# Kernel optimization log

Hardware: AMD Instinct MI355X
Metric: run time of the kernel (lower is better)

The kernel has to match this reference:

```python
import jax, jax.numpy as jnp
import numpy as np

H = W = 512
K = 16          # max instance id (ids 1..K; 0 = background)
N_SIGMA = 1
FG_W = 1.0
W_INST, W_VAR, W_SEED = 1.0, 10.0, 1.0


def _xym(h, w, dtype):
    # torch: linspace(0,1,512) grids, sliced to [:, :h, :w]
    x = jnp.linspace(0.0, 1.0, 512)[:w]
    y = jnp.linspace(0.0, 1.0, 512)[:h]
    xm = jnp.broadcast_to(x[None, :], (h, w))
    ym = jnp.broadcast_to(y[:, None], (h, w))
    return jnp.stack([xm, ym], 0).astype(dtype)  # [2,h,w]


def _lovasz_hinge(logits, labels):
    # logits, labels: flat [P]; labels in {0,1} float
    signs = 2.0 * labels - 1.0
    errors = 1.0 - logits * signs
    perm = jnp.argsort(-errors)           # descending sort
    errors_sorted = errors[perm]
    gt_sorted = labels[perm]
    gts = gt_sorted.sum()
    inter = gts - jnp.cumsum(gt_sorted)
    union = gts + jnp.cumsum(1.0 - gt_sorted)
    jac = 1.0 - inter / union
    grad = jnp.concatenate([jac[:1], jac[1:] - jac[:-1]])
    # lovasz grad is computed from .data (detached) in the torch impl
    return jnp.dot(jax.nn.relu(errors_sorted), jax.lax.stop_gradient(grad))


def _per_instance(mask, spatial_emb, sigma, seed, xym):
    # mask: [H,W] float {0,1}; spatial_emb: [2,H,W]; sigma: [n_sigma,H,W]; seed: [H,W]
    cnt = mask.sum()
    safe = jnp.maximum(cnt, 1.0)
    center = jnp.sum(xym * mask, (1, 2)) / safe                        # [2] (to_center=True)
    s = jnp.sum(sigma * mask, (1, 2)) / safe                           # [n_sigma]
    var = jnp.sum((sigma - jax.lax.stop_gradient(s)[:, None, None]) ** 2 * mask) / (N_SIGMA * safe)
    s_exp = jnp.exp(s * 10.0)
    dist = jnp.exp(-jnp.sum((spatial_emb - center[:, None, None]) ** 2 * s_exp[:, None, None], 0))  # [H,W]
    inst = _lovasz_hinge(dist.ravel() * 2.0 - 1.0, mask.ravel())
    seed_l = FG_W * jnp.sum((seed - jax.lax.stop_gradient(dist)) ** 2 * mask)
    present = cnt > 0
    z = jnp.zeros((), dist.dtype)
    return (jnp.where(present, var, z), jnp.where(present, inst, z),
            jnp.where(present, seed_l, z), present.astype(dist.dtype))


def _per_image(pred, inst, lab, xym):
    spatial_emb = jnp.tanh(pred[0:2]) + xym                            # [2,H,W]
    sigma = pred[2:2 + N_SIGMA]                                        # [n_sigma,H,W]
    seed = jax.nn.sigmoid(pred[2 + N_SIGMA])                           # [H,W]
    ids = jnp.arange(1, K + 1)
    masks = (inst[None] == ids[:, None, None]).astype(pred.dtype)      # [K,H,W]
    var, instl, seedl, pres = jax.vmap(
        _per_instance, in_axes=(0, None, None, None, None))(masks, spatial_emb, sigma, seed, xym)
    obj = pres.sum()
    safe_obj = jnp.maximum(obj, 1.0)
    bg = (lab == 0).astype(pred.dtype)
    seed_total = (jnp.sum(seed ** 2 * bg) + seedl.sum()) / float(H * W)
    return W_INST * instl.sum() / safe_obj + W_VAR * var.sum() / safe_obj + W_SEED * seed_total


def setup_inputs() -> dict:
    key = jax.random.key(0)
    k1, k2, k3 = jax.random.split(key, 3)
    prediction = jax.random.normal(k1, (8, 4, H, W), dtype=jnp.float32)
    instances = jax.random.randint(k2, (8, H, W), 0, K + 1, dtype=jnp.int32)
    labels = jax.random.randint(k3, (8, H, W), 0, 2, dtype=jnp.int32)
    return {"prediction": prediction, "instances": instances, "labels": labels}


def reference(prediction, instances, labels):
    xym = _xym(prediction.shape[2], prediction.shape[3], prediction.dtype)
    losses = jax.vmap(_per_image, in_axes=(0, 0, 0, None))(prediction, instances, labels, xym)
    return losses.mean() + prediction.sum() * 0.0
```

## Files before the change

kernel.cpp:

```cpp
#include <hip/hip_runtime.h>

#define HH 512
#define WW 512
#define NPIX (HH*WW)
#define KK 16
#define BB 8
#define NB 192
#define NBP 200
#define CHS 128
#define CHV 256

__device__ __forceinline__ float fast_rcp(float x){ return __builtin_amdgcn_rcpf(x); }
__device__ __forceinline__ float fast_tanh(float x){
  x = fminf(fmaxf(x, -15.f), 15.f);
  float t = __expf(2.f*x);
  return (t-1.f)*fast_rcp(t+1.f);
}
__device__ __forceinline__ float fast_sigmoid(float x){
  x = fminf(fmaxf(x, -30.f), 30.f);
  return fast_rcp(1.f+__expf(-x));
}

__device__ __forceinline__ float dpp_row_sum16(float v){
  v += __int_as_float(__builtin_amdgcn_update_dpp(0, __float_as_int(v), 0x111, 0xf, 0xf, true));
  v += __int_as_float(__builtin_amdgcn_update_dpp(0, __float_as_int(v), 0x112, 0xf, 0xf, true));
  v += __int_as_float(__builtin_amdgcn_update_dpp(0, __float_as_int(v), 0x114, 0xf, 0xf, true));
  v += __int_as_float(__builtin_amdgcn_update_dpp(0, __float_as_int(v), 0x118, 0xf, 0xf, true));
  return v;
}

__global__ void __launch_bounds__(256) k_sums(
    const float* __restrict__ pred, const int* __restrict__ inst,
    const int* __restrict__ lab, float* __restrict__ partial_s ,
    float* __restrict__ partial_b ) {
  const int bid = blockIdx.x;
  const int b  = bid & 7;
  const int ch = bid >> 3;
  const int tid = threadIdx.x;
  const int wave = tid >> 6, lane = tid & 63;
  __shared__ float lred[KK][16][5];
  __shared__ float lbg[4];
  const float inv = 1.f/511.f;
  const float* ps = pred + (size_t)b*4*NPIX + 2*NPIX;
  const float* pd = ps + NPIX;
  const int*   ib = inst + (size_t)b*NPIX;
  const int*   lb = lab  + (size_t)b*NPIX;
  const int p = ch*2048 + tid*8;
  int4   iv0 = *(const int4*)(ib + p),     iv1 = *(const int4*)(ib + p + 4);
  int4   lv0 = *(const int4*)(lb + p),     lv1 = *(const int4*)(lb + p + 4);
  float4 sv0 = *(const float4*)(ps + p),   sv1 = *(const float4*)(ps + p + 4);
  float4 dv0 = *(const float4*)(pd + p),   dv1 = *(const float4*)(pd + p + 4);
  const float ym  = (float)(p >> 9) * inv;
  const float xm0 = (float)(p & (WW-1)) * inv;
  int   ida[8] = {iv0.x, iv0.y, iv0.z, iv0.w, iv1.x, iv1.y, iv1.z, iv1.w};
  int   laa[8] = {lv0.x, lv0.y, lv0.z, lv0.w, lv1.x, lv1.y, lv1.z, lv1.w};
  float sga[8] = {sv0.x, sv0.y, sv0.z, sv0.w, sv1.x, sv1.y, sv1.z, sv1.w};
  float sda[8] = {dv0.x, dv0.y, dv0.z, dv0.w, dv1.x, dv1.y, dv1.z, dv1.w};
  float xja[8], sg2[8];
  #pragma unroll
  for (int j = 0; j < 8; ++j) {
    xja[j] = xm0 + (float)j*inv;
    sg2[j] = sga[j]*sga[j];
  }

  float sbg = 0.f;
  #pragma unroll
  for (int j = 0; j < 8; ++j)
    if (laa[j] == 0) { float sd = fast_sigmoid(sda[j]); sbg += sd*sd; }
  #pragma unroll
  for (int off = 32; off; off >>= 1) sbg += __shfl_down(sbg, off);
  if (lane == 0) lbg[wave] = sbg;

  #pragma unroll
  for (int k = 0; k < KK; ++k) {
    float c = 0.f, sx = 0.f, ss = 0.f, sq = 0.f;
    #pragma unroll
    for (int j = 0; j < 8; ++j) {
      float m = (ida[j] == k+1) ? 1.f : 0.f;
      c  += m;
      sx = fmaf(m, xja[j], sx);
      ss = fmaf(m, sga[j], ss);
      sq = fmaf(m, sg2[j], sq);
    }
    float sy = c * ym;
    c  = dpp_row_sum16(c);
    sx = dpp_row_sum16(sx);
    sy = dpp_row_sum16(sy);
    ss = dpp_row_sum16(ss);
    sq = dpp_row_sum16(sq);
    if ((lane & 15) == 15) {
      int g = wave*4 + (lane >> 4);
      lred[k][g][0] = c;  lred[k][g][1] = sx; lred[k][g][2] = sy;
      lred[k][g][3] = ss; lred[k][g][4] = sq;
    }
  }
  __syncthreads();
  if (tid < KK) {
    #pragma unroll
    for (int comp = 0; comp < 5; ++comp) {
      float a = 0.f;
      #pragma unroll
      for (int g = 0; g < 16; ++g) a += lred[tid][g][comp];
      partial_s[((size_t)b*80 + tid*5 + comp)*CHS + ch] = a;
    }
  }
  if (tid == 64) partial_b[bid] = lbg[0] + lbg[1] + lbg[2] + lbg[3];
}

__global__ void __launch_bounds__(128) k_reduce(
    const float* __restrict__ partial_s, float* __restrict__ der) {
  const int seg = blockIdx.x;
  const int b = seg >> 4, k = seg & 15;
  const int tid = threadIdx.x;
  const int w = tid >> 6, l = tid & 63;
  __shared__ float red5[5][2];
  #pragma unroll
  for (int comp = 0; comp < 5; ++comp) {
    const float* row = partial_s + ((size_t)b*80 + k*5 + comp)*CHS;
    float a = row[tid];
    #pragma unroll
    for (int off = 32; off; off >>= 1) a += __shfl_down(a, off);
    if (l == 0) red5[comp][w] = a;
  }
  __syncthreads();
  if (tid == 0) {
    float cnt = red5[0][0]+red5[0][1];
    float sx  = red5[1][0]+red5[1][1];
    float sy  = red5[2][0]+red5[2][1];
    float ss  = red5[3][0]+red5[3][1];
    float sq  = red5[4][0]+red5[4][1];
    float safe = fmaxf(cnt, 1.f);
    float rs = fast_rcp(safe);
    float sb = ss*rs;
    float* dd = der + seg*8;
    dd[0] = sx*rs; dd[1] = sy*rs;
    dd[2] = __expf(10.f*sb);
    dd[3] = (cnt > 0.f) ? 1.f : 0.f;
    dd[4] = sb;
    dd[5] = cnt;
    dd[6] = sq - cnt*sb*sb;
  }
}

__global__ void __launch_bounds__(256, 4) k_hist(
    const float* __restrict__ pred, const int* __restrict__ inst,
    const float* __restrict__ der, unsigned int* __restrict__ hist,
    float* __restrict__ partial_v ) {
  const int bid = blockIdx.x;
  const int b  = bid & 7;
  const int ch = bid >> 3;
  const int tid = threadIdx.x;
  const int g = tid >> 4, l4 = tid & 15;
  __shared__ unsigned int lh[KK][NBP];
  __shared__ float sder[KK][4];
  __shared__ float lsl[4];
  if (tid < KK) {
    const float* dd = der + (b*KK + tid)*8;
    sder[tid][0] = dd[0]; sder[tid][1] = dd[1]; sder[tid][2] = dd[2];
  }
  for (int i = tid; i < KK*NBP; i += 256) ((unsigned int*)lh)[i] = 0u;
  __syncthreads();
  float cxa[KK], cya[KK], sea[KK];
  #pragma unroll
  for (int k = 0; k < KK; ++k) {
    cxa[k] = sder[k][0]; cya[k] = sder[k][1]; sea[k] = sder[k][2];
  }
  const float inv = 1.f/511.f;
  const float* pbx = pred + (size_t)b*4*NPIX;
  const float* pby = pbx + NPIX;
  const float* pbd = pbx + 3*NPIX;
  const int*   ib  = inst + (size_t)b*NPIX;
  const int p = ch*1024 + g*64 + l4*4;
  float4 px = *(const float4*)(pbx + p);
  float4 py = *(const float4*)(pby + p);
  int4   iv = *(const int4*)(ib + p);
  float4 dv = *(const float4*)(pbd + p);
  const float ym  = (float)(p >> 9) * inv;
  const float xm0 = (float)(p & (WW-1)) * inv;
  float pxa[4] = {px.x, px.y, px.z, px.w};
  float pya[4] = {py.x, py.y, py.z, py.w};
  int   ida[4] = {iv.x, iv.y, iv.z, iv.w};
  float sda[4] = {dv.x, dv.y, dv.z, dv.w};
  float sloss = 0.f;
  #pragma unroll
  for (int j = 0; j < 4; ++j) {
    float sex = fast_tanh(pxa[j]) + xm0 + (float)j*inv;
    float sey = fast_tanh(pya[j]) + ym;
    int id = ida[j];
    float down = 0.f;
    #pragma unroll
    for (int k = 0; k < KK; ++k) {
      float dx = sex - cxa[k], dy = sey - cya[k];
      float d = __expf(-sea[k]*(dx*dx + dy*dy));
      bool fg = (id == k+1);
      float u  = fg ? (1.f - d) : d;
      int bkt = (int)(u * (float)NB);
      bkt = bkt < (NB-1) ? bkt : (NB-1);
      atomicAdd(&lh[k][bkt], fg ? 0x10001u : 1u);
      down = fg ? d : down;
    }
    if (id >= 1) {
      float dsee = fast_sigmoid(sda[j]) - down;
      sloss = fmaf(dsee, dsee, sloss);
    }
  }
  __syncthreads();
  #pragma unroll
  for (int k = 0; k < KK; ++k) {
    unsigned int* gh = hist + ((size_t)(b*KK + k)*CHV + ch)*NB;
    if (tid < NB) gh[tid] = lh[k][tid];
  }
  #pragma unroll
  for (int off = 32; off; off >>= 1) sloss += __shfl_down(sloss, off);
  if ((tid & 63) == 0) lsl[tid >> 6] = sloss;
  __syncthreads();
  if (tid == 0) partial_v[bid] = lsl[0] + lsl[1] + lsl[2] + lsl[3];
}

__global__ void __launch_bounds__(256) k_lovasz(
    const unsigned int* __restrict__ hist, const float* __restrict__ der,
    const float* __restrict__ partial_v, const float* __restrict__ partial_b,
    float* __restrict__ instl, unsigned int* __restrict__ done,
    float* __restrict__ out) {
  const int seg = blockIdx.x;
  const int tid = threadIdx.x;
  __shared__ float nbL[NB], fbL[NB];
  __shared__ unsigned int sOld;
  const float gts = der[seg*8 + 5];
  const unsigned int* h = hist + (size_t)seg*CHV*NB;
  if (tid < NB) {
    unsigned int nlo = 0, nhi = 0;
    #pragma unroll 8
    for (int c = 0; c < CHV; ++c) {
      unsigned int v = h[(size_t)c*NB + tid];
      nlo += v & 0xffffu; nhi += v >> 16;
    }
    nbL[tid] = (float)nlo; fbL[tid] = (float)nhi;
  }
  __syncthreads();
  if (tid < 64) {
    const int lane = tid;
    float lsum = 0.f;
    if (gts > 0.f) {
      float carryN = 0.f, carryF = 0.f;
      #pragma unroll
      for (int it = 0; it < NB/64; ++it) {
        int bkt = NB - 1 - (it*64 + lane);
        float nb = nbL[bkt], fb = fbL[bkt];
        float sn = nb, sf = fb;
        #pragma unroll
        for (int off = 1; off < 64; off <<= 1) {
          float tn = __shfl_up(sn, off);
          float tf = __shfl_up(sf, off);
          if (lane >= off) { sn += tn; sf += tf; }
        }
        float Nb = carryN + sn - nb;
        float Fb = carryF + sf - fb;
        if (nb > 0.f) {
          float e  = ((float)bkt + 0.5f) * (2.0f/(float)NB);
          float j0 = 1.f - (gts - Fb) / (gts + Nb - Fb);
          float N1 = Nb + nb, F1 = Fb + fb;
          float j1 = 1.f - (gts - F1) / (gts + N1 - F1);
          lsum += e * (j1 - j0);
        }
        carryN += __shfl(sn, 63);
        carryF += __shfl(sf, 63);
      }
      #pragma unroll
      for (int off = 32; off; off >>= 1) lsum += __shfl_down(lsum, off);
    }
    if (lane == 0) {
      instl[seg] = lsum;
      __threadfence();
      sOld = atomicAdd(done, 1u);
    }
  }
  __syncthreads();
  if ((sOld & 127u) != 127u) return;
  __threadfence();
  __shared__ float vtmp[256], btmp[256];
  {
    const int b8 = tid >> 5, j = tid & 31;
    float a = 0.f, c = 0.f;
    #pragma unroll
    for (int i = 0; i < 8; ++i) a += partial_v[(size_t)(j + 32*i)*8 + b8];
    #pragma unroll
    for (int i = 0; i < 4; ++i) c += partial_b[(size_t)(j + 32*i)*8 + b8];
    vtmp[tid] = a; btmp[tid] = c;
  }
  __syncthreads();
  float myv = 0.f;
  if (tid < BB) {
    int b = tid;
    float svl = 0.f, sbg = 0.f;
    #pragma unroll
    for (int j = 0; j < 32; ++j) { svl += vtmp[b*32 + j]; sbg += btmp[b*32 + j]; }
    float obj = 0.f, il = 0.f, vr = 0.f;
    for (int k = 0; k < KK; ++k) {
      int s2 = b*KK + k;
      float cnt = der[s2*8 + 5];
      if (cnt > 0.f) {
        obj += 1.f;
        il  += instl[s2];
        vr  += der[s2*8 + 6] / cnt;
      }
    }
    float so = fmaxf(obj, 1.f);
    myv = il/so + 10.f*vr/so + (sbg + svl)/(float)NPIX;
  }
  #pragma unroll
  for (int off = 4; off; off >>= 1) myv += __shfl_down(myv, off);
  if (tid == 0) out[0] = myv * (1.f/(float)BB);
}

extern "C" void kernel_launch(void* const* d_in, const int* in_sizes, int n_in,
                              void* d_out, int out_size, void* d_ws, size_t ws_size,
                              hipStream_t stream) {
  const float* pred = (const float*)d_in[0];
  const int*   inst = (const int*)d_in[1];
  const int*   lab  = (const int*)d_in[2];
  float* out = (float*)d_out;

  float* der        = (float*)d_ws;
  float* instl      = (float*)((char*)d_ws + 4160);
  unsigned int* done= (unsigned int*)((char*)d_ws + 4736);
  float* partial_b  = (float*)((char*)d_ws + 8192);
  float* partial_v  = (float*)((char*)d_ws + 16384);
  float* partial_s  = (float*)((char*)d_ws + 24576);
  unsigned int* hist= (unsigned int*)((char*)d_ws + 679936);

  k_sums  <<<BB*CHS, 256, 0, stream>>>(pred, inst, lab, partial_s, partial_b);
  k_reduce<<<BB*KK, 128, 0, stream>>>(partial_s, der);
  k_hist  <<<BB*CHV, 256, 0, stream>>>(pred, inst, der, hist, partial_v);
  k_lovasz<<<BB*KK, 256, 0, stream>>>(hist, der, partial_v, partial_b,
                                      instl, done, out);
}
```

Baseline: 61.17 us.

## Fuse reduce into sums via last-block, atomically merge histograms, algebraic exp2 distance

The per-instance reduction kernel is folded into k_sums: the last block to finish, detected with an atomic counter, computes the derived centers and scales, which removes one launch. Per-block histograms are no longer written out in full. k_hist instead merges non-zero bins into one global 64-bit histogram per segment with atomics, and that histogram is zeroed inside k_sums. The lovasz kernel therefore reads 192 bins per segment instead of reducing 256 chunks. The distance exponent is expanded into precomputed coefficients with exp2, and bucketing uses a pre-scaled value. The risks are atomic contention, a serial last-block reduction over 128 chunks, and small numeric differences from the expanded quadratic.

```diff
diff --git a/kernel.cpp b/kernel.cpp
--- a/kernel.cpp
+++ b/kernel.cpp
@@ -32,7 +32,9 @@
 __global__ void __launch_bounds__(256) k_sums(
     const float* __restrict__ pred, const int* __restrict__ inst,
     const int* __restrict__ lab, float* __restrict__ partial_s ,
-    float* __restrict__ partial_b ) {
+    float* __restrict__ partial_b ,
+    unsigned long long* __restrict__ hist64, unsigned int* __restrict__ done2,
+    float* __restrict__ der) {
   const int bid = blockIdx.x;
   const int b  = bid & 7;
   const int ch = bid >> 3;
@@ -40,6 +42,8 @@
   const int wave = tid >> 6, lane = tid & 63;
   __shared__ float lred[KK][16][5];
   __shared__ float lbg[4];
+  __shared__ unsigned int sOld2;
+  if (tid < 48) ((unsigned int*)hist64)[bid*48 + tid] = 0u;
   const float inv = 1.f/511.f;
   const float* ps = pred + (size_t)b*4*NPIX + 2*NPIX;
   const float* pd = ps + NPIX;
@@ -105,46 +109,38 @@
     }
   }
   if (tid == 64) partial_b[bid] = lbg[0] + lbg[1] + lbg[2] + lbg[3];
-}
-
-__global__ void __launch_bounds__(128) k_reduce(
-    const float* __restrict__ partial_s, float* __restrict__ der) {
-  const int seg = blockIdx.x;
-  const int b = seg >> 4, k = seg & 15;
-  const int tid = threadIdx.x;
-  const int w = tid >> 6, l = tid & 63;
-  __shared__ float red5[5][2];
-  #pragma unroll
-  for (int comp = 0; comp < 5; ++comp) {
-    const float* row = partial_s + ((size_t)b*80 + k*5 + comp)*CHS;
-    float a = row[tid];
-    #pragma unroll
-    for (int off = 32; off; off >>= 1) a += __shfl_down(a, off);
-    if (l == 0) red5[comp][w] = a;
-  }
-  __syncthreads();
-  if (tid == 0) {
-    float cnt = red5[0][0]+red5[0][1];
-    float sx  = red5[1][0]+red5[1][1];
-    float sy  = red5[2][0]+red5[2][1];
-    float ss  = red5[3][0]+red5[3][1];
-    float sq  = red5[4][0]+red5[4][1];
+  __syncthreads();
+  if (tid == 0) { __threadfence(); sOld2 = atomicAdd(done2, 1u); }
+  __syncthreads();
+  if ((sOld2 & 1023u) != 1023u) return;
+  __threadfence();
+  if (tid < 128) {
+    const int seg = tid, b2 = seg >> 4, k2 = seg & 15;
+    float acc[5];
+    #pragma unroll
+    for (int comp = 0; comp < 5; ++comp) {
+      const float* row = partial_s + ((size_t)b2*80 + k2*5 + comp)*CHS;
+      float a = 0.f;
+      for (int c2 = 0; c2 < CHS; ++c2) a += row[c2];
+      acc[comp] = a;
+    }
+    float cnt = acc[0];
     float safe = fmaxf(cnt, 1.f);
     float rs = fast_rcp(safe);
-    float sb = ss*rs;
+    float sb = acc[3]*rs;
     float* dd = der + seg*8;
-    dd[0] = sx*rs; dd[1] = sy*rs;
+    dd[0] = acc[1]*rs; dd[1] = acc[2]*rs;
     dd[2] = __expf(10.f*sb);
     dd[3] = (cnt > 0.f) ? 1.f : 0.f;
     dd[4] = sb;
     dd[5] = cnt;
-    dd[6] = sq - cnt*sb*sb;
+    dd[6] = acc[4] - cnt*sb*sb;
   }
 }
 
 __global__ void __launch_bounds__(256, 4) k_hist(
     const float* __restrict__ pred, const int* __restrict__ inst,
-    const float* __restrict__ der, unsigned int* __restrict__ hist,
+    const float* __restrict__ der, unsigned long long* __restrict__ hist64,
     float* __restrict__ partial_v ) {
   const int bid = blockIdx.x;
   const int b  = bid & 7;
@@ -160,10 +156,16 @@
   }
   for (int i = tid; i < KK*NBP; i += 256) ((unsigned int*)lh)[i] = 0u;
   __syncthreads();
-  float cxa[KK], cya[KK], sea[KK];
+  const float L2E = 1.4426950408889634f;
+  float seaL[KK], AL[KK], BL[KK], CL[KK];
   #pragma unroll
   for (int k = 0; k < KK; ++k) {
-    cxa[k] = sder[k][0]; cya[k] = sder[k][1]; sea[k] = sder[k][2];
+    float cx = sder[k][0], cy = sder[k][1], se = sder[k][2];
+    float seL = se * L2E;
+    seaL[k] = -seL;
+    AL[k] = 2.f*cx*seL;
+    BL[k] = 2.f*cy*seL;
+    CL[k] = -(cx*cx + cy*cy)*seL;
   }
   const float inv = 1.f/511.f;
   const float* pbx = pred + (size_t)b*4*NPIX;
@@ -186,15 +188,17 @@
   for (int j = 0; j < 4; ++j) {
     float sex = fast_tanh(pxa[j]) + xm0 + (float)j*inv;
     float sey = fast_tanh(pya[j]) + ym;
+    float s2 = fmaf(sex, sex, sey*sey);
     int id = ida[j];
     float down = 0.f;
     #pragma unroll
     for (int k = 0; k < KK; ++k) {
-      float dx = sex - cxa[k], dy = sey - cya[k];
-      float d = __expf(-sea[k]*(dx*dx + dy*dy));
+      float t2 = fmaf(seaL[k], s2, fmaf(AL[k], sex, fmaf(BL[k], sey, CL[k])));
+      float d = __builtin_amdgcn_exp2f(t2);
       bool fg = (id == k+1);
-      float u  = fg ? (1.f - d) : d;
-      int bkt = (int)(u * (float)NB);
+      float dN = d * (float)NB;
+      float uN = fg ? ((float)NB - dN) : dN;
+      int bkt = (int)uN;
       bkt = bkt < (NB-1) ? bkt : (NB-1);
       atomicAdd(&lh[k][bkt], fg ? 0x10001u : 1u);
       down = fg ? d : down;
@@ -207,8 +211,14 @@
   __syncthreads();
   #pragma unroll
   for (int k = 0; k < KK; ++k) {
-    unsigned int* gh = hist + ((size_t)(b*KK + k)*CHV + ch)*NB;
-    if (tid < NB) gh[tid] = lh[k][tid];
+    if (tid < NB) {
+      unsigned int v = lh[k][tid];
+      if (v) {
+        unsigned long long add = (unsigned long long)(v & 0xffffu)
+                               | ((unsigned long long)(v >> 16) << 32);
+        atomicAdd(&hist64[(size_t)(b*KK + k)*NB + tid], add);
+      }
+    }
   }
   #pragma unroll
   for (int off = 32; off; off >>= 1) sloss += __shfl_down(sloss, off);
@@ -218,26 +228,15 @@
 }
 
 __global__ void __launch_bounds__(256) k_lovasz(
-    const unsigned int* __restrict__ hist, const float* __restrict__ der,
+    const unsigned long long* __restrict__ hist64, const float* __restrict__ der,
     const float* __restrict__ partial_v, const float* __restrict__ partial_b,
     float* __restrict__ instl, unsigned int* __restrict__ done,
     float* __restrict__ out) {
   const int seg = blockIdx.x;
   const int tid = threadIdx.x;
-  __shared__ float nbL[NB], fbL[NB];
   __shared__ unsigned int sOld;
   const float gts = der[seg*8 + 5];
-  const unsigned int* h = hist + (size_t)seg*CHV*NB;
-  if (tid < NB) {
-    unsigned int nlo = 0, nhi = 0;
-    #pragma unroll 8
-    for (int c = 0; c < CHV; ++c) {
-      unsigned int v = h[(size_t)c*NB + tid];
-      nlo += v & 0xffffu; nhi += v >> 16;
-    }
-    nbL[tid] = (float)nlo; fbL[tid] = (float)nhi;
-  }
-  __syncthreads();
+  const unsigned long long* h = hist64 + (size_t)seg*NB;
   if (tid < 64) {
     const int lane = tid;
     float lsum = 0.f;
@@ -246,7 +245,9 @@
       #pragma unroll
       for (int it = 0; it < NB/64; ++it) {
         int bkt = NB - 1 - (it*64 + lane);
-        float nb = nbL[bkt], fb = fbL[bkt];
+        unsigned long long v = h[bkt];
+        float nb = (float)(unsigned int)(v & 0xffffffffu);
+        float fb = (float)(unsigned int)(v >> 32);
         float sn = nb, sf = fb;
         #pragma unroll
         for (int off = 1; off < 64; off <<= 1) {
@@ -321,17 +322,18 @@
   const int*   lab  = (const int*)d_in[2];
   float* out = (float*)d_out;
 
-  float* der        = (float*)d_ws;
-  float* instl      = (float*)((char*)d_ws + 4160);
-  unsigned int* done= (unsigned int*)((char*)d_ws + 4736);
-  float* partial_b  = (float*)((char*)d_ws + 8192);
-  float* partial_v  = (float*)((char*)d_ws + 16384);
-  float* partial_s  = (float*)((char*)d_ws + 24576);
-  unsigned int* hist= (unsigned int*)((char*)d_ws + 679936);
-
-  k_sums  <<<BB*CHS, 256, 0, stream>>>(pred, inst, lab, partial_s, partial_b);
-  k_reduce<<<BB*KK, 128, 0, stream>>>(partial_s, der);
-  k_hist  <<<BB*CHV, 256, 0, stream>>>(pred, inst, der, hist, partial_v);
-  k_lovasz<<<BB*KK, 256, 0, stream>>>(hist, der, partial_v, partial_b,
+  float* der         = (float*)d_ws;
+  float* instl       = (float*)((char*)d_ws + 4160);
+  unsigned int* done = (unsigned int*)((char*)d_ws + 4736);
+  unsigned int* done2= (unsigned int*)((char*)d_ws + 4740);
+  float* partial_b   = (float*)((char*)d_ws + 8192);
+  float* partial_v   = (float*)((char*)d_ws + 16384);
+  float* partial_s   = (float*)((char*)d_ws + 24576);
+  unsigned long long* hist64 = (unsigned long long*)((char*)d_ws + 360448);
+
+  k_sums  <<<BB*CHS, 256, 0, stream>>>(pred, inst, lab, partial_s, partial_b,
+                                       hist64, done2, der);
+  k_hist  <<<BB*CHV, 256, 0, stream>>>(pred, inst, der, hist64, partial_v);
+  k_lovasz<<<BB*KK, 256, 0, stream>>>(hist64, der, partial_v, partial_b,
                                       instl, done, out);
 }
```

New measurement: 111.3 us. 82.0% more time.

## Halve histogram chunk count and expand Gaussian distance into precomputed exp2 form

Applied to the files above, without the earlier changes.

The histogram kernel now processes 8 pixels per thread over 128 chunks instead of 4 pixels over 256, which halves the per-block histogram zeroing and global histogram writes and the number of partial histograms the Lovasz kernel must merge. The squared distance is expanded algebraically into a per-instance quadratic in the embedding, with log2(e) folded in so a raw exp2 replaces __expf. The bucket index scaling is also folded into the distance computation. The trade-offs are fewer blocks for parallelism and some loss of floating-point accuracy from the expanded quadratic, which could shift bucket assignments slightly.

```diff
diff --git a/kernel.cpp b/kernel.cpp
--- a/kernel.cpp
+++ b/kernel.cpp
@@ -8,7 +8,7 @@
 #define NB 192
 #define NBP 200
 #define CHS 128
-#define CHV 256
+#define CHV 128
 
 __device__ __forceinline__ float fast_rcp(float x){ return __builtin_amdgcn_rcpf(x); }
 __device__ __forceinline__ float fast_tanh(float x){
@@ -160,48 +160,60 @@
   }
   for (int i = tid; i < KK*NBP; i += 256) ((unsigned int*)lh)[i] = 0u;
   __syncthreads();
-  float cxa[KK], cya[KK], sea[KK];
+  const float L2E = 1.4426950408889634f;
+  float seaL[KK], AL[KK], BL[KK], CL[KK];
   #pragma unroll
   for (int k = 0; k < KK; ++k) {
-    cxa[k] = sder[k][0]; cya[k] = sder[k][1]; sea[k] = sder[k][2];
+    float cx = sder[k][0], cy = sder[k][1], se = sder[k][2];
+    float seL = se * L2E;
+    seaL[k] = -seL;
+    AL[k] = 2.f*cx*seL;
+    BL[k] = 2.f*cy*seL;
+    CL[k] = -(cx*cx + cy*cy)*seL;
   }
   const float inv = 1.f/511.f;
   const float* pbx = pred + (size_t)b*4*NPIX;
   const float* pby = pbx + NPIX;
   const float* pbd = pbx + 3*NPIX;
   const int*   ib  = inst + (size_t)b*NPIX;
-  const int p = ch*1024 + g*64 + l4*4;
-  float4 px = *(const float4*)(pbx + p);
-  float4 py = *(const float4*)(pby + p);
-  int4   iv = *(const int4*)(ib + p);
-  float4 dv = *(const float4*)(pbd + p);
-  const float ym  = (float)(p >> 9) * inv;
-  const float xm0 = (float)(p & (WW-1)) * inv;
-  float pxa[4] = {px.x, px.y, px.z, px.w};
-  float pya[4] = {py.x, py.y, py.z, py.w};
-  int   ida[4] = {iv.x, iv.y, iv.z, iv.w};
-  float sda[4] = {dv.x, dv.y, dv.z, dv.w};
+  const int base = ch*2048 + g*128;
   float sloss = 0.f;
   #pragma unroll
-  for (int j = 0; j < 4; ++j) {
-    float sex = fast_tanh(pxa[j]) + xm0 + (float)j*inv;
-    float sey = fast_tanh(pya[j]) + ym;
-    int id = ida[j];
-    float down = 0.f;
-    #pragma unroll
-    for (int k = 0; k < KK; ++k) {
-      float dx = sex - cxa[k], dy = sey - cya[k];
-      float d = __expf(-sea[k]*(dx*dx + dy*dy));
-      bool fg = (id == k+1);
-      float u  = fg ? (1.f - d) : d;
-      int bkt = (int)(u * (float)NB);
-      bkt = bkt < (NB-1) ? bkt : (NB-1);
-      atomicAdd(&lh[k][bkt], fg ? 0x10001u : 1u);
-      down = fg ? d : down;
-    }
-    if (id >= 1) {
-      float dsee = fast_sigmoid(sda[j]) - down;
-      sloss = fmaf(dsee, dsee, sloss);
+  for (int it = 0; it < 2; ++it) {
+    const int p = base + it*64 + l4*4;
+    float4 px = *(const float4*)(pbx + p);
+    float4 py = *(const float4*)(pby + p);
+    int4   iv = *(const int4*)(ib + p);
+    float4 dv = *(const float4*)(pbd + p);
+    const float ym  = (float)(p >> 9) * inv;
+    const float xm0 = (float)(p & (WW-1)) * inv;
+    float pxa[4] = {px.x, px.y, px.z, px.w};
+    float pya[4] = {py.x, py.y, py.z, py.w};
+    int   ida[4] = {iv.x, iv.y, iv.z, iv.w};
+    float sda[4] = {dv.x, dv.y, dv.z, dv.w};
+    #pragma unroll
+    for (int j = 0; j < 4; ++j) {
+      float sex = fast_tanh(pxa[j]) + xm0 + (float)j*inv;
+      float sey = fast_tanh(pya[j]) + ym;
+      float s2 = fmaf(sex, sex, sey*sey);
+      int id = ida[j];
+      float down = 0.f;
+      #pragma unroll
+      for (int k = 0; k < KK; ++k) {
+        float t2 = fmaf(seaL[k], s2, fmaf(AL[k], sex, fmaf(BL[k], sey, CL[k])));
+        float d = __builtin_amdgcn_exp2f(t2);
+        bool fg = (id == k+1);
+        float dN = d * (float)NB;
+        float uN = fg ? ((float)NB - dN) : dN;
+        int bkt = (int)uN;
+        bkt = bkt < (NB-1) ? bkt : (NB-1);
+        atomicAdd(&lh[k][bkt], fg ? 0x10001u : 1u);
+        down = fg ? d : down;
+      }
+      if (id >= 1) {
+        float dsee = fast_sigmoid(sda[j]) - down;
+        sloss = fmaf(dsee, dsee, sloss);
+      }
     }
   }
   __syncthreads();
@@ -283,9 +295,10 @@
     const int b8 = tid >> 5, j = tid & 31;
     float a = 0.f, c = 0.f;
     #pragma unroll
-    for (int i = 0; i < 8; ++i) a += partial_v[(size_t)(j + 32*i)*8 + b8];
-    #pragma unroll
-    for (int i = 0; i < 4; ++i) c += partial_b[(size_t)(j + 32*i)*8 + b8];
+    for (int i = 0; i < 4; ++i) {
+      a += partial_v[(size_t)(j + 32*i)*8 + b8];
+      c += partial_b[(size_t)(j + 32*i)*8 + b8];
+    }
     vtmp[tid] = a; btmp[tid] = c;
   }
   __syncthreads();
@@ -321,13 +334,13 @@
   const int*   lab  = (const int*)d_in[2];
   float* out = (float*)d_out;
 
-  float* der        = (float*)d_ws;
-  float* instl      = (float*)((char*)d_ws + 4160);
-  unsigned int* done= (unsigned int*)((char*)d_ws + 4736);
-  float* partial_b  = (float*)((char*)d_ws + 8192);
-  float* partial_v  = (float*)((char*)d_ws + 16384);
-  float* partial_s  = (float*)((char*)d_ws + 24576);
-  unsigned int* hist= (unsigned int*)((char*)d_ws + 679936);
+  float* der         = (float*)d_ws;
+  float* instl       = (float*)((char*)d_ws + 4160);
+  unsigned int* done = (unsigned int*)((char*)d_ws + 4736);
+  float* partial_b   = (float*)((char*)d_ws + 8192);
+  float* partial_v   = (float*)((char*)d_ws + 16384);
+  float* partial_s   = (float*)((char*)d_ws + 24576);
+  unsigned int* hist = (unsigned int*)((char*)d_ws + 679936);
 
   k_sums  <<<BB*CHS, 256, 0, stream>>>(pred, inst, lab, partial_s, partial_b);
   k_reduce<<<BB*KK, 128, 0, stream>>>(partial_s, der);
```

After: 55.69 us. -9.0%, faster.
